# Kernel tuning notes

Measured on AMD Instinct MI355X. Metric: run time of the kernel, lower is better.

Reference implementation:

```python
import jax, jax.numpy as jnp
import numpy as np

N_NODES = 100000
N_EDGES = 1000000
IN_DIM = 128
OUT_DIM = 64
NEG_SLOPE = 0.2


def setup_inputs() -> dict:
    key = jax.random.key(0)
    k = jax.random.split(key, 6)
    h = jax.random.normal(k[0], (N_NODES, IN_DIM), dtype=jnp.float32)
    # xavier-uniform-ish scales for linear weights
    W_w = jax.random.uniform(k[1], (OUT_DIM, IN_DIM), dtype=jnp.float32,
                             minval=-1.0, maxval=1.0) * np.sqrt(6.0 / (IN_DIM + OUT_DIM))
    W_b = jnp.zeros((OUT_DIM,), dtype=jnp.float32)
    a_w = jax.random.uniform(k[2], (1, 2 * OUT_DIM), dtype=jnp.float32,
                             minval=-1.0, maxval=1.0) * np.sqrt(6.0 / (2 * OUT_DIM + 1))
    a_b = jnp.zeros((1,), dtype=jnp.float32)
    edge_index = jax.random.randint(k[3], (2, N_EDGES), 0, N_NODES, dtype=jnp.int64)
    return {"h": h, "W_w": W_w, "W_b": W_b, "a_w": a_w, "a_b": a_b,
            "edge_index": edge_index}


def reference(h, W_w, W_b, a_w, a_b, edge_index):
    # Wh = W(h): [N, D_out]
    Wh = h @ W_w.T + W_b
    src, tgt = edge_index[0], edge_index[1]
    D = Wh.shape[1]
    # a([e_src, e_tgt]) decomposes: score = Wh@a_src per-node + Wh@a_tgt per-node,
    # gathered by edge (avoids materializing the [E, 2D] concat).
    s_src = Wh @ a_w[0, :D]   # [N]
    s_tgt = Wh @ a_w[0, D:]   # [N]
    logits = jax.nn.leaky_relu(s_src[src] + s_tgt[tgt] + a_b[0], NEG_SLOPE)  # [E]
    # NOTE: global softmax over all edges (dim=0), faithful to the source.
    attn = jax.nn.softmax(logits, axis=0)
    e_src = Wh[src]  # [E, D] gather
    messages = jnp.zeros_like(Wh).at[tgt].add(attn[:, None] * e_src)  # scatter-add
    return jax.nn.leaky_relu(messages, NEG_SLOPE)
```

## Files before the change

kernel.cpp:

```cpp
#include <hip/hip_runtime.h>
#include <math.h>

#define N_NODES 100000
#define N_EDGES 1000000
#define IN_DIM  128
#define OUT_DIM 64
#define NEG     0.2f

#define SCAN_BLOCKS 391
#define EDGE_BLOCKS 3907

#define G_GROUPS 32
#define EPG      (N_EDGES / G_GROUPS)
#define CHUNK_N  25000
#define HIST_BLOCKS (G_GROUPS * 4)

typedef __attribute__((ext_vector_type(8))) short short8;
typedef __attribute__((ext_vector_type(4))) float f32x4;

#define MFMA(A, B, C) __builtin_amdgcn_mfma_f32_16x16x32_bf16(A, B, C, 0, 0, 0)

union U16 { unsigned u[4]; short8 s; };

__device__ __forceinline__ void split8(const float* x, short8& hi, short8& lo) {
    U16 H, L;
#pragma unroll
    for (int i = 0; i < 4; ++i) {
        float a = x[2 * i], b = x[2 * i + 1];
        unsigned ua = __float_as_uint(a), ub = __float_as_uint(b);
        unsigned ha = ua & 0xffff0000u, hb = ub & 0xffff0000u;
        H.u[i] = (ua >> 16) | hb;
        float la = a - __uint_as_float(ha);
        float lb = b - __uint_as_float(hb);
        L.u[i] = (__float_as_uint(la) >> 16) | (__float_as_uint(lb) & 0xffff0000u);
    }
    hi = H.s; lo = L.s;
}

__device__ __forceinline__ unsigned pk2(float a, float b) {
    unsigned ua = __float_as_uint(a); ua = (ua + 0x7fffu + ((ua >> 16) & 1u)) >> 16;
    unsigned ub = __float_as_uint(b); ub = (ub + 0x7fffu + ((ub >> 16) & 1u)) >> 16;
    return ua | (ub << 16);
}

__global__ __launch_bounds__(256, 3) void k1_mfma(
    const float* __restrict__ h, const float* __restrict__ W,
    const float* __restrict__ Wb, const float* __restrict__ aw,
    unsigned short* __restrict__ Whb, float* __restrict__ s_src,
    float* __restrict__ s_tgt)
{
    __shared__ float4 smem4[2176];
    unsigned short* wfh = (unsigned short*)smem4;
    unsigned short* wfl = wfh + 8192;

    const int tid  = threadIdx.x;
    const int lane = tid & 63, w = tid >> 6;
    const int c = lane & 15, g = lane >> 4;
    const int n0 = blockIdx.x * 128;

#pragma unroll
    for (int it = 0; it < 4; ++it) {
        int U = tid + 256 * it;
        int pos = U >> 6, l = U & 63;
        int nb = pos >> 2, ks = pos & 3;
        int r  = 16 * nb + (l & 15);
        int k0 = 32 * ks + 8 * (l >> 4);
        float a[8];
        *(float4*)&a[0] = *(const float4*)(W + r * IN_DIM + k0);
        *(float4*)&a[4] = *(const float4*)(W + r * IN_DIM + k0 + 4);
        short8 hi, lo; split8(a, hi, lo);
        *(short8*)(wfh + (size_t)U * 8) = hi;
        *(short8*)(wfl + (size_t)U * 8) = lo;
    }
    __syncthreads();

    const int na0 = n0 + 32 * w + c;
    const float* hp0 = h + (size_t)min(na0, N_NODES - 1) * IN_DIM + 8 * g;
    const float* hp1 = h + (size_t)min(na0 + 16, N_NODES - 1) * IN_DIM + 8 * g;

    f32x4 acc[2][4];
    {
        f32x4 z = {0.f, 0.f, 0.f, 0.f};
#pragma unroll
        for (int m = 0; m < 2; ++m)
#pragma unroll
            for (int nb = 0; nb < 4; ++nb) acc[m][nb] = z;
    }

#pragma unroll 2
    for (int ks = 0; ks < 4; ++ks) {
        short8 bh[4], bl[4];
#pragma unroll
        for (int nb = 0; nb < 4; ++nb) {
            int u = ((nb * 4 + ks) * 64 + lane) * 8;
            bh[nb] = *(const short8*)(wfh + u);
            bl[nb] = *(const short8*)(wfl + u);
        }
        float am[8];
        short8 ah, al;
        *(float4*)&am[0] = *(const float4*)(hp0 + 32 * ks);
        *(float4*)&am[4] = *(const float4*)(hp0 + 32 * ks + 4);
        split8(am, ah, al);
#pragma unroll
        for (int nb = 0; nb < 4; ++nb) {
            acc[0][nb] = MFMA(ah, bh[nb], acc[0][nb]);
            acc[0][nb] = MFMA(ah, bl[nb], acc[0][nb]);
            acc[0][nb] = MFMA(al, bh[nb], acc[0][nb]);
        }
        *(float4*)&am[0] = *(const float4*)(hp1 + 32 * ks);
        *(float4*)&am[4] = *(const float4*)(hp1 + 32 * ks + 4);
        split8(am, ah, al);
#pragma unroll
        for (int nb = 0; nb < 4; ++nb) {
            acc[1][nb] = MFMA(ah, bh[nb], acc[1][nb]);
            acc[1][nb] = MFMA(ah, bl[nb], acc[1][nb]);
            acc[1][nb] = MFMA(al, bh[nb], acc[1][nb]);
        }
    }

    float wb[4], w1[4], w2[4];
#pragma unroll
    for (int nb = 0; nb < 4; ++nb) {
        wb[nb] = Wb[16 * nb + c];
        w1[nb] = aw[16 * nb + c];
        w2[nb] = aw[OUT_DIM + 16 * nb + c];
    }
#pragma unroll
    for (int m = 0; m < 2; ++m)
#pragma unroll
        for (int r = 0; r < 4; ++r) {
            float s1 = 0.f, s2 = 0.f;
#pragma unroll
            for (int nb = 0; nb < 4; ++nb) {
                float v = acc[m][nb][r] + wb[nb];
                acc[m][nb][r] = v;
                s1 = fmaf(v, w1[nb], s1);
                s2 = fmaf(v, w2[nb], s2);
            }
#pragma unroll
            for (int mk = 1; mk < 16; mk <<= 1) {
                s1 += __shfl_xor(s1, mk);
                s2 += __shfl_xor(s2, mk);
            }
            if (c == 0) {
                int node = n0 + 32 * w + 16 * m + 4 * g + r;
                if (node < N_NODES) { s_src[node] = s1; s_tgt[node] = s2; }
            }
        }

    __syncthreads();
    float* tr = (float*)smem4;
#pragma unroll
    for (int m = 0; m < 2; ++m)
#pragma unroll
        for (int nb = 0; nb < 4; ++nb)
#pragma unroll
            for (int r = 0; r < 4; ++r)
                tr[(32 * w + 16 * m + 4 * g + r) * 68 + 16 * nb + c] = acc[m][nb][r];
    __syncthreads();

#pragma unroll
    for (int j = 0; j < 4; ++j) {
        int idx = tid + 256 * j;
        int nloc = idx >> 3, q = idx & 7;
        int node = n0 + nloc;
        if (node < N_NODES) {
            const float* r8 = &tr[nloc * 68 + q * 8];
            uint4 u;
            u.x = pk2(r8[0], r8[1]); u.y = pk2(r8[2], r8[3]);
            u.z = pk2(r8[4], r8[5]); u.w = pk2(r8[6], r8[7]);
            ((uint4*)Whb)[(size_t)node * 8 + q] = u;
        }
    }
}

__global__ __launch_bounds__(256) void k_hist(
    const int* __restrict__ ei, unsigned char* __restrict__ deg_g8,
    unsigned* __restrict__ rank)
{
    __shared__ unsigned cnt[CHUNK_N];
    const int g  = blockIdx.x >> 2;
    const int c0 = (blockIdx.x & 3) * CHUNK_N;
    const int tid = threadIdx.x;

    for (int i = tid; i < CHUNK_N; i += 256) cnt[i] = 0u;
    __syncthreads();

    const int ebase = g * EPG;
    const int2* tp2 = (const int2*)(ei + N_EDGES + ebase);
#pragma unroll 4
    for (int i = tid; i < EPG / 2; i += 256) {
        int2 tv = tp2[i];
        int e0 = ebase + 2 * i;
        unsigned u0 = (unsigned)(tv.x - c0), u1 = (unsigned)(tv.y - c0);
        if (u0 < CHUNK_N) rank[e0]     = atomicAdd(&cnt[u0], 1u);
        if (u1 < CHUNK_N) rank[e0 + 1] = atomicAdd(&cnt[u1], 1u);
    }
    __syncthreads();

    unsigned* dg = (unsigned*)(deg_g8 + (size_t)g * N_NODES + c0);
    for (int i = tid; i < CHUNK_N / 4; i += 256) {
        unsigned v = cnt[4 * i] | (cnt[4 * i + 1] << 8) |
                     (cnt[4 * i + 2] << 16) | (cnt[4 * i + 3] << 24);
        dg[i] = v;
    }
}

__global__ __launch_bounds__(256) void k_scanA(
    const unsigned char* __restrict__ deg_g8, unsigned* __restrict__ psum)
{
    const int i = blockIdx.x * 256 + threadIdx.x;
    unsigned v = 0;
    if (i < N_NODES) {
#pragma unroll
        for (int x = 0; x < G_GROUPS; ++x)
            v += deg_g8[(size_t)x * N_NODES + i];
    }
#pragma unroll
    for (int off = 32; off; off >>= 1) v += __shfl_xor(v, off);
    __shared__ unsigned us[4];
    if ((threadIdx.x & 63) == 0) us[threadIdx.x >> 6] = v;
    __syncthreads();
    if (threadIdx.x == 0) psum[blockIdx.x] = us[0] + us[1] + us[2] + us[3];
}

__global__ __launch_bounds__(256) void k_scan3(
    const unsigned char* __restrict__ deg_g8, const unsigned* __restrict__ psum,
    unsigned* __restrict__ row, unsigned* __restrict__ row_g)
{
    __shared__ unsigned sc[256];
    __shared__ unsigned ps[4];
    const int t = threadIdx.x;
    const int i = blockIdx.x * 256 + t;

    unsigned pv = 0;
    if (t < blockIdx.x) pv = psum[t];
    if (t + 256 < blockIdx.x) pv += psum[t + 256];
#pragma unroll
    for (int off = 32; off; off >>= 1) pv += __shfl_xor(pv, off);
    if ((t & 63) == 0) ps[t >> 6] = pv;

    unsigned d[G_GROUPS];
    unsigned tot = 0;
    if (i < N_NODES) {
#pragma unroll
        for (int x = 0; x < G_GROUPS; ++x) {
            d[x] = deg_g8[(size_t)x * N_NODES + i];
            tot += d[x];
        }
    }
    sc[t] = tot;
    __syncthreads();
    for (int off = 1; off < 256; off <<= 1) {
        unsigned u = (t >= off) ? sc[t - off] : 0u;
        __syncthreads();
        sc[t] += u;
        __syncthreads();
    }
    const unsigned bb = ps[0] + ps[1] + ps[2] + ps[3];
    if (i < N_NODES) {
        unsigned base = bb + sc[t] - tot;
        row[i] = base;
        unsigned run = base;
#pragma unroll
        for (int x = 0; x < G_GROUPS; ++x) {
            row_g[(size_t)x * N_NODES + i] = run;
            run += d[x];
        }
    }
    if (i == 0) row[N_NODES] = N_EDGES;
}

__global__ __launch_bounds__(256) void k_fill(
    const int* __restrict__ ei, const float* __restrict__ s_src,
    const float* __restrict__ s_tgt, const float* __restrict__ ab,
    const unsigned* __restrict__ rank, const unsigned* __restrict__ row_g,
    int* __restrict__ bin, float* __restrict__ bsum)
{
    const float ab0 = ab[0];
    float lsum = 0.f;
    const int e = blockIdx.x * 256 + threadIdx.x;
    if (e < N_EDGES) {
        int s = ei[e], t = ei[N_EDGES + e];
        float x = s_src[s] + s_tgt[t] + ab0;
        float l = x > 0.f ? x : NEG * x;
        lsum = __expf(l);
        int g = e / EPG;
        unsigned pos = row_g[(size_t)g * N_NODES + t] + rank[e];
        bin[pos] = s;
    }
#pragma unroll
    for (int off = 32; off; off >>= 1) lsum += __shfl_xor(lsum, off);
    __shared__ float ssum[4];
    if ((threadIdx.x & 63) == 0) ssum[threadIdx.x >> 6] = lsum;
    __syncthreads();
    if (threadIdx.x == 0)
        bsum[blockIdx.x] = ssum[0] + ssum[1] + ssum[2] + ssum[3];
}

__global__ __launch_bounds__(512) void k_gsum(
    const float* __restrict__ bsum, float* __restrict__ gsum)
{
    __shared__ float sf[8];
    const int t = threadIdx.x;
    float s = 0.f;
    for (int i = t; i < EDGE_BLOCKS; i += 512) s += bsum[i];
#pragma unroll
    for (int off = 32; off; off >>= 1) s += __shfl_xor(s, off);
    if ((t & 63) == 0) sf[t >> 6] = s;
    __syncthreads();
    if (t == 0) {
        float tot = 0.f;
#pragma unroll
        for (int i = 0; i < 8; ++i) tot += sf[i];
        gsum[0] = tot;
    }
}

__global__ __launch_bounds__(256) void k_gather(
    const unsigned* __restrict__ row, const int* __restrict__ bin,
    const float* __restrict__ gsum, const float* __restrict__ s_src,
    const float* __restrict__ s_tgt, const float* __restrict__ ab,
    const unsigned short* __restrict__ Whb, float* __restrict__ out)
{
    const int lane = threadIdx.x & 63;
    const int t = blockIdx.x * 4 + (threadIdx.x >> 6);
    if (t >= N_NODES) return;
    const float stt = s_tgt[t];
    const float ab0 = ab[0];
    const unsigned beg = row[t], end = row[t + 1];
    float a0 = 0.f, a1 = 0.f, a2 = 0.f, a3 = 0.f;
    for (unsigned base = beg; base < end; base += 64) {
        const int cnt = (int)min(64u, end - base);
        int p = 0;
        if (lane < cnt) p = bin[base + lane];
        float x = s_src[p] + stt + ab0;
        float wl = __expf(x > 0.f ? x : NEG * x);
        int j = 0;
        for (; j + 4 <= cnt; j += 4) {
            int   s0 = __shfl(p, j);     float w0 = __shfl(wl, j);
            int   s1 = __shfl(p, j + 1); float w1 = __shfl(wl, j + 1);
            int   s2 = __shfl(p, j + 2); float w2 = __shfl(wl, j + 2);
            int   s3 = __shfl(p, j + 3); float w3 = __shfl(wl, j + 3);
            float v0 = __uint_as_float((unsigned)Whb[(size_t)s0 * OUT_DIM + lane] << 16);
            float v1 = __uint_as_float((unsigned)Whb[(size_t)s1 * OUT_DIM + lane] << 16);
            float v2 = __uint_as_float((unsigned)Whb[(size_t)s2 * OUT_DIM + lane] << 16);
            float v3 = __uint_as_float((unsigned)Whb[(size_t)s3 * OUT_DIM + lane] << 16);
            a0 = fmaf(w0, v0, a0);
            a1 = fmaf(w1, v1, a1);
            a2 = fmaf(w2, v2, a2);
            a3 = fmaf(w3, v3, a3);
        }
        for (; j < cnt; ++j) {
            int   s = __shfl(p, j);
            float w = __shfl(wl, j);
            float v = __uint_as_float((unsigned)Whb[(size_t)s * OUT_DIM + lane] << 16);
            a0 = fmaf(w, v, a0);
        }
    }
    float v = ((a0 + a1) + (a2 + a3)) * (1.0f / gsum[0]);
    out[(size_t)t * OUT_DIM + lane] = v > 0.f ? v : NEG * v;
}

extern "C" void kernel_launch(void* const* d_in, const int* in_sizes, int n_in,
                              void* d_out, int out_size, void* d_ws, size_t ws_size,
                              hipStream_t stream)
{
    const float* h  = (const float*)d_in[0];
    const float* W  = (const float*)d_in[1];
    const float* Wb = (const float*)d_in[2];
    const float* aw = (const float*)d_in[3];
    const float* ab = (const float*)d_in[4];
    const int*   ei = (const int*)d_in[5];

    unsigned short* Whb = (unsigned short*)d_ws;
    float* s_src   = (float*)(Whb + (size_t)N_NODES * OUT_DIM);
    float* s_tgt   = s_src + N_NODES;
    unsigned char* deg_g8 = (unsigned char*)(s_tgt + N_NODES);
    unsigned* row    = (unsigned*)(deg_g8 + (size_t)G_GROUPS * N_NODES);
    unsigned* row_g  = row + N_NODES + 1;
    unsigned* psum   = row_g + (size_t)G_GROUPS * N_NODES;
    unsigned* rank   = psum + 512;
    int*      bin    = (int*)(rank + N_EDGES);
    float*    bsum   = (float*)(bin + N_EDGES);
    float*    gsum   = bsum + 4096;

    float* out = (float*)d_out;

    k_hist<<<HIST_BLOCKS, 256, 0, stream>>>(ei, deg_g8, rank);
    k1_mfma<<<(N_NODES + 127) / 128, 256, 0, stream>>>(h, W, Wb, aw, Whb,
                                                       s_src, s_tgt);
    k_scanA<<<SCAN_BLOCKS, 256, 0, stream>>>(deg_g8, psum);
    k_scan3<<<SCAN_BLOCKS, 256, 0, stream>>>(deg_g8, psum, row, row_g);
    k_fill<<<EDGE_BLOCKS, 256, 0, stream>>>(ei, s_src, s_tgt, ab, rank,
                                            row_g, bin, bsum);
    k_gsum<<<1, 512, 0, stream>>>(bsum, gsum);
    k_gather<<<(N_NODES + 3) / 4, 256, 0, stream>>>(row, bin, gsum, s_src,
                                                    s_tgt, ab, Whb, out);
}
```

Measured before the change: 224.9 us.

## Store edge weights with CSR bins and gather four edges per wave with vector loads

The fill kernel now writes each edge's exp-logit next to its source index in the CSR bin, so the gather kernel no longer re-reads s_src per edge or recomputes the exponential. The gather is restructured so each wave handles four edges at once: each 16-lane quarter loads 8-byte ushort4 chunks of a source row, and a cross-lane shuffle reduction combines the quarters at the end. This is meant to cut the random s_src gathers and issue fewer, wider memory requests. In exchange the bin array doubles in size, the final reduction and output store are more complex, and the output store pattern becomes strided within each quarter.

Result: faster. 213.4 us (-5.1%).

```diff
diff --git a/kernel.cpp b/kernel.cpp
--- a/kernel.cpp
+++ b/kernel.cpp
@@ -275,7 +275,7 @@
     const int* __restrict__ ei, const float* __restrict__ s_src,
     const float* __restrict__ s_tgt, const float* __restrict__ ab,
     const unsigned* __restrict__ rank, const unsigned* __restrict__ row_g,
-    int* __restrict__ bin, float* __restrict__ bsum)
+    int2* __restrict__ bin, float* __restrict__ bsum)
 {
     const float ab0 = ab[0];
     float lsum = 0.f;
@@ -284,10 +284,11 @@
         int s = ei[e], t = ei[N_EDGES + e];
         float x = s_src[s] + s_tgt[t] + ab0;
         float l = x > 0.f ? x : NEG * x;
-        lsum = __expf(l);
+        float ex = __expf(l);
+        lsum = ex;
         int g = e / EPG;
         unsigned pos = row_g[(size_t)g * N_NODES + t] + rank[e];
-        bin[pos] = s;
+        bin[pos] = make_int2(s, __float_as_int(ex));
     }
 #pragma unroll
     for (int off = 32; off; off >>= 1) lsum += __shfl_xor(lsum, off);
@@ -318,48 +319,43 @@
 }
 
 __global__ __launch_bounds__(256) void k_gather(
-    const unsigned* __restrict__ row, const int* __restrict__ bin,
-    const float* __restrict__ gsum, const float* __restrict__ s_src,
-    const float* __restrict__ s_tgt, const float* __restrict__ ab,
-    const unsigned short* __restrict__ Whb, float* __restrict__ out)
+    const unsigned* __restrict__ row, const int2* __restrict__ bin,
+    const float* __restrict__ gsum, const unsigned short* __restrict__ Whb,
+    float* __restrict__ out)
 {
     const int lane = threadIdx.x & 63;
     const int t = blockIdx.x * 4 + (threadIdx.x >> 6);
     if (t >= N_NODES) return;
-    const float stt = s_tgt[t];
-    const float ab0 = ab[0];
+    const int q = lane >> 4, sub = lane & 15;
     const unsigned beg = row[t], end = row[t + 1];
-    float a0 = 0.f, a1 = 0.f, a2 = 0.f, a3 = 0.f;
+
+    float ax = 0.f, ay = 0.f, az = 0.f, aw_ = 0.f;
+
     for (unsigned base = beg; base < end; base += 64) {
         const int cnt = (int)min(64u, end - base);
-        int p = 0;
-        if (lane < cnt) p = bin[base + lane];
-        float x = s_src[p] + stt + ab0;
-        float wl = __expf(x > 0.f ? x : NEG * x);
-        int j = 0;
-        for (; j + 4 <= cnt; j += 4) {
-            int   s0 = __shfl(p, j);     float w0 = __shfl(wl, j);
-            int   s1 = __shfl(p, j + 1); float w1 = __shfl(wl, j + 1);
-            int   s2 = __shfl(p, j + 2); float w2 = __shfl(wl, j + 2);
-            int   s3 = __shfl(p, j + 3); float w3 = __shfl(wl, j + 3);
-            float v0 = __uint_as_float((unsigned)Whb[(size_t)s0 * OUT_DIM + lane] << 16);
-            float v1 = __uint_as_float((unsigned)Whb[(size_t)s1 * OUT_DIM + lane] << 16);
-            float v2 = __uint_as_float((unsigned)Whb[(size_t)s2 * OUT_DIM + lane] << 16);
-            float v3 = __uint_as_float((unsigned)Whb[(size_t)s3 * OUT_DIM + lane] << 16);
-            a0 = fmaf(w0, v0, a0);
-            a1 = fmaf(w1, v1, a1);
-            a2 = fmaf(w2, v2, a2);
-            a3 = fmaf(w3, v3, a3);
-        }
-        for (; j < cnt; ++j) {
-            int   s = __shfl(p, j);
-            float w = __shfl(wl, j);
-            float v = __uint_as_float((unsigned)Whb[(size_t)s * OUT_DIM + lane] << 16);
-            a0 = fmaf(w, v, a0);
-        }
-    }
-    float v = ((a0 + a1) + (a2 + a3)) * (1.0f / gsum[0]);
-    out[(size_t)t * OUT_DIM + lane] = v > 0.f ? v : NEG * v;
+        int2 pw = make_int2(0, 0);
+        if (lane < cnt) pw = bin[base + lane];
+        for (int j = 0; j < cnt; j += 4) {
+            int   s = __shfl(pw.x, j + q);
+            float w = __int_as_float(__shfl(pw.y, j + q));
+            ushort4 v = *(const ushort4*)(Whb + (size_t)s * OUT_DIM + 4 * sub);
+            ax  = fmaf(w, __uint_as_float((unsigned)v.x << 16), ax);
+            ay  = fmaf(w, __uint_as_float((unsigned)v.y << 16), ay);
+            az  = fmaf(w, __uint_as_float((unsigned)v.z << 16), az);
+            aw_ = fmaf(w, __uint_as_float((unsigned)v.w << 16), aw_);
+        }
+    }
+
+    ax  += __shfl_xor(ax, 16);  ax  += __shfl_xor(ax, 32);
+    ay  += __shfl_xor(ay, 16);  ay  += __shfl_xor(ay, 32);
+    az  += __shfl_xor(az, 16);  az  += __shfl_xor(az, 32);
+    aw_ += __shfl_xor(aw_, 16); aw_ += __shfl_xor(aw_, 32);
+
+    const float inv = 1.0f / gsum[0];
+    float r = (q == 0) ? ax : (q == 1) ? ay : (q == 2) ? az : aw_;
+    r *= inv;
+    r = r > 0.f ? r : NEG * r;
+    out[(size_t)t * OUT_DIM + 4 * sub + q] = r;
 }
 
 extern "C" void kernel_launch(void* const* d_in, const int* in_sizes, int n_in,
@@ -374,16 +370,16 @@
     const int*   ei = (const int*)d_in[5];
 
     unsigned short* Whb = (unsigned short*)d_ws;
-    float* s_src   = (float*)(Whb + (size_t)N_NODES * OUT_DIM);
-    float* s_tgt   = s_src + N_NODES;
+    int2*  bin   = (int2*)(Whb + (size_t)N_NODES * OUT_DIM);
+    float* s_src = (float*)(bin + N_EDGES);
+    float* s_tgt = s_src + N_NODES;
     unsigned char* deg_g8 = (unsigned char*)(s_tgt + N_NODES);
-    unsigned* row    = (unsigned*)(deg_g8 + (size_t)G_GROUPS * N_NODES);
-    unsigned* row_g  = row + N_NODES + 1;
-    unsigned* psum   = row_g + (size_t)G_GROUPS * N_NODES;
-    unsigned* rank   = psum + 512;
-    int*      bin    = (int*)(rank + N_EDGES);
-    float*    bsum   = (float*)(bin + N_EDGES);
-    float*    gsum   = bsum + 4096;
+    unsigned* row   = (unsigned*)(deg_g8 + (size_t)G_GROUPS * N_NODES);
+    unsigned* row_g = row + N_NODES + 1;
+    unsigned* psum  = row_g + (size_t)G_GROUPS * N_NODES;
+    unsigned* rank  = psum + 512;
+    float* bsum  = (float*)(rank + N_EDGES);
+    float* gsum  = bsum + 4096;
 
     float* out = (float*)d_out;
 
@@ -395,6 +391,5 @@
     k_fill<<<EDGE_BLOCKS, 256, 0, stream>>>(ei, s_src, s_tgt, ab, rank,
                                             row_g, bin, bsum);
     k_gsum<<<1, 512, 0, stream>>>(bsum, gsum);
-    k_gather<<<(N_NODES + 3) / 4, 256, 0, stream>>>(row, bin, gsum, s_src,
-                                                    s_tgt, ab, Whb, out);
-}
+    k_gather<<<(N_NODES + 3) / 4, 256, 0, stream>>>(row, bin, gsum, Whb, out);
+}
```
